# Optimization experiments

Measured on AMD Instinct MI355X. Metric: run time of the kernel, lower is better.

Reference implementation:

```python
import jax, jax.numpy as jnp
import numpy as np

E, H, L = 512, 1024, 4
VS, VT = 32000, 32000
B, SS, TT = 64, 48, 48
PAD = 0


def _cell(x, h, c, Wih, Whh, bih, bhh):
    # torch.nn.LSTMCell math: gate order i, f, g, o
    g = x @ Wih.T + h @ Whh.T + bih + bhh
    i, f, gg, o = jnp.split(g, 4, axis=-1)
    c = jax.nn.sigmoid(f) * c + jax.nn.sigmoid(i) * jnp.tanh(gg)
    h = jax.nn.sigmoid(o) * jnp.tanh(c)
    return h, c


def setup_inputs() -> dict:
    key = jax.random.key(0)
    ks = jax.random.split(key, 14)
    s = 0.05
    d = {}
    d['src_tokens'] = jax.random.randint(ks[0], (SS, B), 0, VS, dtype=jnp.int32)
    d['tgt_tokens'] = jax.random.randint(ks[1], (TT, B), 0, VT, dtype=jnp.int32)
    d['src_emb'] = jax.random.normal(ks[2], (VS, E)) * s
    d['tgt_emb'] = jax.random.normal(ks[3], (VT, E)) * s
    d['enc_Wih0'] = jax.random.normal(ks[4], (4 * H, E)) * s
    d['enc_WihR'] = jax.random.normal(ks[5], (L - 1, 4 * H, H)) * s
    d['enc_Whh'] = jax.random.normal(ks[6], (L, 4 * H, H)) * s
    d['enc_bih'] = jnp.zeros((L, 4 * H))
    d['enc_bhh'] = jnp.zeros((L, 4 * H))
    d['dec_Wih0'] = jax.random.normal(ks[7], (4 * H, E + H)) * s
    d['dec_WihR'] = jax.random.normal(ks[8], (L - 1, 4 * H, H)) * s
    d['dec_Whh'] = jax.random.normal(ks[9], (L, 4 * H, H)) * s
    d['dec_bih'] = jnp.zeros((L, 4 * H))
    d['dec_bhh'] = jnp.zeros((L, 4 * H))
    d['att_vec_W'] = jax.random.normal(ks[10], (H, 2 * H)) * s
    d['readout_W'] = jax.random.normal(ks[11], (VT, H)) * s
    return d


def _forward(src_tokens, tgt_tokens, src_emb, tgt_emb, enc_Wih0, enc_WihR,
             enc_Whh, enc_bih, enc_bhh, dec_Wih0, dec_WihR, dec_Whh, dec_bih,
             dec_bhh, att_vec_W, readout_W):
    src_x = src_emb[src_tokens]                      # [SS, B, E]
    h0 = jnp.zeros((L, B, H), src_emb.dtype)
    c0 = jnp.zeros((L, B, H), src_emb.dtype)

    def enc_step(carry, x_t):
        h, c = carry
        inp = x_t
        hs, cs = [], []
        for l in range(L):
            Wih = enc_Wih0 if l == 0 else enc_WihR[l - 1]
            hn, cn = _cell(inp, h[l], c[l], Wih, enc_Whh[l], enc_bih[l], enc_bhh[l])
            hs.append(hn); cs.append(cn)
            inp = hn
        return (jnp.stack(hs), jnp.stack(cs)), inp

    (hT, cT), enc_out = jax.lax.scan(enc_step, (h0, c0), src_x)
    src_enc = enc_out.transpose(1, 0, 2)             # [B, SS, H]

    # decoder init: last encoder layer (h, c) copied to every decoder layer
    hd = jnp.tile(hT[-1][None], (L, 1, 1))
    cd = jnp.tile(cT[-1][None], (L, 1, 1))
    tgt_x = tgt_emb[tgt_tokens[:-1]]                 # [TT-1, B, E]
    att0 = jnp.zeros((B, H), src_emb.dtype)

    def dec_step(carry, y_t):
        h, c, att = carry
        inp = jnp.concatenate([y_t, att], axis=-1)   # input feeding
        hs, cs = [], []
        for l in range(L):
            Wih = dec_Wih0 if l == 0 else dec_WihR[l - 1]
            hn, cn = _cell(inp, h[l], c[l], Wih, dec_Whh[l], dec_bih[l], dec_bhh[l])
            hs.append(hn); cs.append(cn)
            inp = hn
        h_top = hs[-1]
        # global attention, 'dot' score (full-length seqs -> all-zero mask is a no-op)
        scores = jnp.einsum('bsh,bh->bs', src_enc, h_top)
        alpha = jax.nn.softmax(scores, axis=-1)
        ctx = jnp.einsum('bs,bsh->bh', alpha, src_enc)
        att_t = jnp.tanh(jnp.concatenate([h_top, ctx], axis=-1) @ att_vec_W.T)
        return (jnp.stack(hs), jnp.stack(cs), att_t), att_t

    _, att_ves = jax.lax.scan(dec_step, (hd, cd, att0), tgt_x)  # [TT-1, B, H]

    logp = jax.nn.log_softmax(att_ves @ readout_W.T, axis=-1)   # [TT-1, B, VT]
    gold = tgt_tokens[1:]
    gold_lp = jnp.take_along_axis(logp, gold[..., None], axis=-1)[..., 0]
    mask = (gold != PAD).astype(logp.dtype)
    return (gold_lp * mask).sum(axis=0)              # [B]


def reference(src_tokens, tgt_tokens, src_emb, tgt_emb, enc_Wih0, enc_WihR,
              enc_Whh, enc_bih, enc_bhh, dec_Wih0, dec_WihR, dec_Whh, dec_bih,
              dec_bhh, att_vec_W, readout_W):
    return _forward(src_tokens, tgt_tokens, src_emb, tgt_emb, enc_Wih0,
                    enc_WihR, enc_Whh, enc_bih, enc_bhh, dec_Wih0, dec_WihR,
                    dec_Whh, dec_bih, dec_bhh, att_vec_W, readout_W)
```

## Files before the change

### kernel.cpp

```cpp
#include <hip/hip_runtime.h>


typedef __attribute__((ext_vector_type(8))) short bf16x8;
typedef __attribute__((ext_vector_type(4))) float f32x4;

#define SMEM_BYTES 32768

__device__ __forceinline__ float bf2f(ushort u) {
  union { uint i; float f; } v; v.i = ((uint)u) << 16; return v.f;
}
__device__ __forceinline__ ushort f2bf(float x) {
  union { float f; uint i; } v; v.f = x;
  uint r = (v.i + 0x7fffu + ((v.i >> 16) & 1u)) >> 16;
  return (ushort)r;
}
__device__ __forceinline__ float sigm(float x) { return 1.f / (1.f + expf(-x)); }

__device__ __forceinline__ void gemm_term(
    const ushort* __restrict__ A, int lda,
    const ushort* __restrict__ W, int ldw,
    int K, int m0, int n0,
    f32x4 acc[4], char* s)
{
  char* sA0 = s;
  char* sB0 = s + 8192;
  char* sA1 = s + 16384;
  char* sB1 = s + 24576;
  const int tid = threadIdx.x;
  const int lane = tid & 63;
  const int w = tid >> 6;
  const int r0 = tid >> 3;
  const int cge = (tid & 7) << 3;
  const ushort* Arow0 = A + (size_t)(m0 + r0) * lda + cge;
  const ushort* Arow1 = A + (size_t)(m0 + r0 + 32) * lda + cge;
  const ushort* Wrow0 = W + (size_t)(n0 + r0) * ldw + cge;
  const ushort* Wrow1 = W + (size_t)(n0 + r0 + 32) * ldw + cge;
  const int so0 = r0 * 128 + (((tid & 7) << 4) ^ ((r0 & 7) << 4));
  const int so1 = so0 + 4096;

  uint4 a0 = *reinterpret_cast<const uint4*>(Arow0);
  uint4 a1 = *reinterpret_cast<const uint4*>(Arow1);
  uint4 b0 = *reinterpret_cast<const uint4*>(Wrow0);
  uint4 b1 = *reinterpret_cast<const uint4*>(Wrow1);
  *reinterpret_cast<uint4*>(sA0 + so0) = a0;
  *reinterpret_cast<uint4*>(sA0 + so1) = a1;
  *reinterpret_cast<uint4*>(sB0 + so0) = b0;
  *reinterpret_cast<uint4*>(sB0 + so1) = b1;
  if (K > 64) {
    a0 = *reinterpret_cast<const uint4*>(Arow0 + 64);
    a1 = *reinterpret_cast<const uint4*>(Arow1 + 64);
    b0 = *reinterpret_cast<const uint4*>(Wrow0 + 64);
    b1 = *reinterpret_cast<const uint4*>(Wrow1 + 64);
  }
  const int axor = (lane & 7) << 4;
  const int arow = (w * 16 + (lane & 15)) * 128;
  const int brow = (lane & 15) * 128;
  const int kb0 = (lane >> 4) << 4;
  for (int kt = 0; kt < K; kt += 64) {
    char* cA = (kt & 64) ? sA1 : sA0;
    char* cB = (kt & 64) ? sB1 : sB0;
    char* nA = (kt & 64) ? sA0 : sA1;
    char* nB = (kt & 64) ? sB0 : sB1;
    __syncthreads();
    if (kt + 64 < K) {
      *reinterpret_cast<uint4*>(nA + so0) = a0;
      *reinterpret_cast<uint4*>(nA + so1) = a1;
      *reinterpret_cast<uint4*>(nB + so0) = b0;
      *reinterpret_cast<uint4*>(nB + so1) = b1;
      if (kt + 128 < K) {
        a0 = *reinterpret_cast<const uint4*>(Arow0 + kt + 128);
        a1 = *reinterpret_cast<const uint4*>(Arow1 + kt + 128);
        b0 = *reinterpret_cast<const uint4*>(Wrow0 + kt + 128);
        b1 = *reinterpret_cast<const uint4*>(Wrow1 + kt + 128);
      }
    }
#pragma unroll
    for (int ks = 0; ks < 2; ++ks) {
      const int kb = ks * 64 + kb0;
      bf16x8 af = *reinterpret_cast<const bf16x8*>(cA + arow + (kb ^ axor));
#pragma unroll
      for (int nf = 0; nf < 4; ++nf) {
        bf16x8 bfr = *reinterpret_cast<const bf16x8*>(
            cB + nf * 2048 + brow + (kb ^ axor));
        acc[nf] = __builtin_amdgcn_mfma_f32_16x16x32_bf16(af, bfr, acc[nf], 0, 0, 0);
      }
    }
  }
  __syncthreads();
}

__device__ __forceinline__ void store_f32(
    float* __restrict__ out, int ldo, int m0, int n0, f32x4 acc[4])
{
  const int tid = threadIdx.x, lane = tid & 63, w = tid >> 6;
  const int rbase = w * 16 + ((lane >> 4) << 2);
  const int cb = lane & 15;
#pragma unroll
  for (int nf = 0; nf < 4; ++nf)
#pragma unroll
    for (int r = 0; r < 4; ++r)
      out[(size_t)(m0 + rbase + r) * ldo + n0 + nf * 16 + cb] = acc[nf][r];
}

__device__ __forceinline__ void cell_store(
    float* smemF, f32x4 acc[4],
    float* __restrict__ c, ushort* __restrict__ hout,
    ushort* __restrict__ senc_t, int j0)
{
  const int tid = threadIdx.x, lane = tid & 63, w = tid >> 6;
  const int rbase = w * 16 + ((lane >> 4) << 2);
  const int cb = lane & 15;
  __syncthreads();
#pragma unroll
  for (int nf = 0; nf < 4; ++nf)
#pragma unroll
    for (int r = 0; r < 4; ++r)
      smemF[(rbase + r) * 68 + nf * 16 + cb] = acc[nf][r];
  __syncthreads();
#pragma unroll
  for (int i = 0; i < 4; ++i) {
    const int id = tid + i * 256;
    const int b = id >> 4, u = id & 15;
    const float g0 = smemF[b * 68 + u * 4 + 0];
    const float g1 = smemF[b * 68 + u * 4 + 1];
    const float g2 = smemF[b * 68 + u * 4 + 2];
    const float g3 = smemF[b * 68 + u * 4 + 3];
    const int off = b * 1024 + j0 + u;
    const float cold = c[off];
    const float ig = sigm(g0), fg = sigm(g1), gg = tanhf(g2), og = sigm(g3);
    const float cn = fg * cold + ig * gg;
    const float hv = og * tanhf(cn);
    c[off] = cn;
    const ushort hb = f2bf(hv);
    hout[off] = hb;
    if (senc_t) senc_t[(size_t)b * 49152 + j0 + u] = hb;
  }
}

__global__ __launch_bounds__(256) void nmt_init(float* c, ushort* henc, ushort* attbf)
{
  const int idx = blockIdx.x * 256 + threadIdx.x;
  if (idx < 262144) c[idx] = 0.f;
  if (idx < 65536) {
    attbf[idx] = 0;
    henc[idx] = 0;
    henc[(size_t)1 * 49 * 65536 + idx] = 0;
    henc[(size_t)2 * 49 * 65536 + idx] = 0;
    henc[(size_t)3 * 49 * 65536 + idx] = 0;
  }
}

__global__ __launch_bounds__(256) void nmt_convperm(
    const float* __restrict__ in, ushort* __restrict__ out,
    int L, int Kin, int col0, int Kout)
{
  const size_t idx = (size_t)blockIdx.x * 256 + threadIdx.x;
  const size_t total = (size_t)L * 4096 * Kout;
  if (idx >= total) return;
  const int k = (int)(idx % Kout);
  const size_t rem = idx / Kout;
  const int rp = (int)(rem % 4096);
  const int l = (int)(rem / 4096);
  const int j = rp >> 2, g = rp & 3;
  out[idx] = f2bf(in[((size_t)l * 4096 + g * 1024 + j) * Kin + col0 + k]);
}

__global__ __launch_bounds__(256) void nmt_convplain(
    const float* __restrict__ in, ushort* __restrict__ out, size_t n)
{
  const size_t idx = (size_t)blockIdx.x * 256 + threadIdx.x;
  if (idx < n) out[idx] = f2bf(in[idx]);
}

__global__ __launch_bounds__(256) void nmt_bias(
    const float* __restrict__ bih, const float* __restrict__ bhh, float* __restrict__ bc)
{
  const int idx = blockIdx.x * 256 + threadIdx.x;
  if (idx >= 4 * 4096) return;
  const int rp = idx & 4095, l = idx >> 12;
  const int j = rp >> 2, g = rp & 3;
  bc[idx] = bih[l * 4096 + g * 1024 + j] + bhh[l * 4096 + g * 1024 + j];
}

__global__ __launch_bounds__(256) void nmt_gather(
    const int* __restrict__ tok, const float* __restrict__ emb,
    ushort* __restrict__ out, int rows)
{
  const size_t idx = (size_t)blockIdx.x * 256 + threadIdx.x;
  if (idx >= (size_t)rows * 512) return;
  const int k = (int)(idx & 511);
  const int r = (int)(idx >> 9);
  out[idx] = f2bf(emb[(size_t)tok[r] * 512 + k]);
}

__global__ __launch_bounds__(256) void nmt_pre(
    const ushort* __restrict__ A, const ushort* __restrict__ Wp,
    const float* __restrict__ bc0, float* __restrict__ out, int K)
{
  __shared__ __align__(16) char smem[SMEM_BYTES];
  const int m0 = blockIdx.x * 64, n0 = blockIdx.y * 64;
  const int lane = threadIdx.x & 63;
  const int cb = lane & 15;
  f32x4 acc[4];
#pragma unroll
  for (int nf = 0; nf < 4; ++nf) {
    const float bv = bc0[n0 + nf * 16 + cb];
#pragma unroll
    for (int r = 0; r < 4; ++r) acc[nf][r] = bv;
  }
  gemm_term(A, K, Wp, K, K, m0, n0, acc, smem);
  store_f32(out, 4096, m0, n0, acc);
}

__global__ __launch_bounds__(256) void nmt_decinit(
    const ushort* __restrict__ henc, float* c, ushort* h)
{
  const int idx = blockIdx.x * 256 + threadIdx.x;
  if (idx >= 65536) return;
  const ushort hv = henc[((size_t)3 * 49 + 48) * 65536 + idx];
  const float cv = c[3 * 65536 + idx];
  c[idx] = cv; c[65536 + idx] = cv; c[2 * 65536 + idx] = cv;
  h[idx] = hv; h[65536 + idx] = hv; h[2 * 65536 + idx] = hv; h[3 * 65536 + idx] = hv;
}

__global__ __launch_bounds__(256) void nmt_sv(
    const ushort* __restrict__ senc, const ushort* __restrict__ attW,
    ushort* __restrict__ SV)
{
  __shared__ __align__(16) char smem[SMEM_BYTES];
  const int b = blockIdx.x;
  const int n0 = blockIdx.y * 64;
  const int tid = threadIdx.x, lane = tid & 63, w = tid >> 6;
  const int rbase = w * 16 + ((lane >> 4) << 2), cb = lane & 15;
  f32x4 acc[4];
#pragma unroll
  for (int nf = 0; nf < 4; ++nf)
#pragma unroll
    for (int r = 0; r < 4; ++r) acc[nf][r] = 0.f;
  gemm_term(senc + (size_t)b * 49152, 1024, attW + 1024, 2048, 1024, 0, n0,
            acc, smem);
#pragma unroll
  for (int nf = 0; nf < 4; ++nf)
#pragma unroll
    for (int r = 0; r < 4; ++r) {
      const int row = rbase + r;
      if (row < 48)
        SV[(size_t)b * 49152 + row * 1024 + n0 + nf * 16 + cb] = f2bf(acc[nf][r]);
    }
}

__global__ __launch_bounds__(256) void nmt_enc_cell(
    int u, int lo, ushort* __restrict__ henc, ushort* __restrict__ srcenc,
    float* __restrict__ c,
    const ushort* __restrict__ WihR, const ushort* __restrict__ Whh,
    const float* __restrict__ X0, const float* __restrict__ bcE)
{
  __shared__ __align__(16) char smem[SMEM_BYTES];
  const int l = lo + blockIdx.y;
  const int t = u - l;
  const int n0 = blockIdx.x * 64;
  const int tid = threadIdx.x, lane = tid & 63, w = tid >> 6;
  const int rbase = w * 16 + ((lane >> 4) << 2), cb = lane & 15;
  f32x4 acc[4];
  if (l == 0) {
#pragma unroll
    for (int nf = 0; nf < 4; ++nf)
#pragma unroll
      for (int r = 0; r < 4; ++r)
        acc[nf][r] = X0[(size_t)t * 262144 + (size_t)(rbase + r) * 4096 + n0 + nf * 16 + cb];
  } else {
#pragma unroll
    for (int nf = 0; nf < 4; ++nf) {
      const float bv = bcE[l * 4096 + n0 + nf * 16 + cb];
#pragma unroll
      for (int r = 0; r < 4; ++r) acc[nf][r] = bv;
    }
    gemm_term(henc + ((size_t)(l - 1) * 49 + t + 1) * 65536, 1024,
              WihR + (size_t)(l - 1) * 4194304, 1024, 1024, 0, n0, acc, smem);
  }
  gemm_term(henc + ((size_t)l * 49 + t) * 65536, 1024,
            Whh + (size_t)l * 4194304, 1024, 1024, 0, n0, acc, smem);
  cell_store((float*)smem, acc, c + l * 65536,
             henc + ((size_t)l * 49 + t + 1) * 65536,
             (l == 3) ? (srcenc + t * 1024) : (ushort*)nullptr, n0 >> 2);
}

__global__ __launch_bounds__(256) void nmt_dec_stage(
    int l, const ushort* __restrict__ hp, ushort* __restrict__ hn,
    float* __restrict__ c,
    const ushort* __restrict__ Whh, const ushort* __restrict__ WihR,
    const ushort* __restrict__ Wd0a, const ushort* __restrict__ attbf,
    const float* __restrict__ Y0t, const float* __restrict__ bcD,
    float* __restrict__ pbuf)
{
  __shared__ __align__(16) char smem[SMEM_BYTES];
  const int n0 = blockIdx.x * 64;
  const int tid = threadIdx.x, lane = tid & 63, w = tid >> 6;
  const int rbase = w * 16 + ((lane >> 4) << 2), cb = lane & 15;
  f32x4 acc[4];
  if (blockIdx.y == 0) {
    if (l == 0) {
#pragma unroll
      for (int nf = 0; nf < 4; ++nf)
#pragma unroll
        for (int r = 0; r < 4; ++r) {
          const size_t o = (size_t)(rbase + r) * 4096 + n0 + nf * 16 + cb;
          acc[nf][r] = Y0t[o] + pbuf[o];
        }
      gemm_term(attbf, 1024, Wd0a, 1024, 1024, 0, n0, acc, smem);
    } else {
#pragma unroll
      for (int nf = 0; nf < 4; ++nf)
#pragma unroll
        for (int r = 0; r < 4; ++r)
          acc[nf][r] = pbuf[(size_t)l * 262144 + (size_t)(rbase + r) * 4096 + n0 + nf * 16 + cb];
      gemm_term(hn + (l - 1) * 65536, 1024, WihR + (size_t)(l - 1) * 4194304,
                1024, 1024, 0, n0, acc, smem);
    }
    cell_store((float*)smem, acc, c + l * 65536, hn + l * 65536,
               (ushort*)nullptr, n0 >> 2);
  } else {
    const int lp = (l + 1) & 3;
    if (lp == 0) {
#pragma unroll
      for (int nf = 0; nf < 4; ++nf)
#pragma unroll
        for (int r = 0; r < 4; ++r) acc[nf][r] = 0.f;
      gemm_term(hn, 1024, Whh, 1024, 1024, 0, n0, acc, smem);
    } else {
#pragma unroll
      for (int nf = 0; nf < 4; ++nf) {
        const float bv = bcD[lp * 4096 + n0 + nf * 16 + cb];
#pragma unroll
        for (int r = 0; r < 4; ++r) acc[nf][r] = bv;
      }
      gemm_term(hp + lp * 65536, 1024, Whh + (size_t)lp * 4194304,
                1024, 1024, 0, n0, acc, smem);
    }
    store_f32(pbuf + (size_t)lp * 262144, 4096, 0, n0, acc);
  }
}

__global__ __launch_bounds__(256) void nmt_partial0(
    const ushort* __restrict__ h0, const ushort* __restrict__ Whh0,
    float* __restrict__ pbuf)
{
  __shared__ __align__(16) char smem[SMEM_BYTES];
  const int n0 = blockIdx.x * 64;
  f32x4 acc[4];
#pragma unroll
  for (int nf = 0; nf < 4; ++nf)
#pragma unroll
    for (int r = 0; r < 4; ++r) acc[nf][r] = 0.f;
  gemm_term(h0, 1024, Whh0, 1024, 1024, 0, n0, acc, smem);
  store_f32(pbuf, 4096, 0, n0, acc);
}

__global__ __launch_bounds__(256) void nmt_attnAB(
    const ushort* __restrict__ h3, const ushort* __restrict__ senc,
    const ushort* __restrict__ SV, const ushort* __restrict__ attW,
    float* __restrict__ ctx2, float* __restrict__ hb)
{
  __shared__ __align__(16) char smem[SMEM_BYTES];
  const int bid = blockIdx.x;
  const int tid = threadIdx.x, lane = tid & 63, w = tid >> 6;
  if (bid < 64) {
    float* sc = (float*)smem;
    float* al = (float*)smem + 64;
    const int b = bid;
    const ushort* sb = senc + (size_t)b * 49152;
    const ushort* vb = SV + (size_t)b * 49152;
    float hreg[16];
#pragma unroll
    for (int q = 0; q < 16; ++q) hreg[q] = bf2f(h3[b * 1024 + lane * 16 + q]);
    for (int s = w; s < 48; s += 4) {
      const ushort* vr = sb + s * 1024 + lane * 16;
      float p = 0.f;
#pragma unroll
      for (int q = 0; q < 16; ++q) p += bf2f(vr[q]) * hreg[q];
      for (int d = 1; d < 64; d <<= 1) p += __shfl_xor(p, d);
      if (lane == 0) sc[s] = p;
    }
    __syncthreads();
    if (tid < 64) {
      const float v = (lane < 48) ? sc[lane] : -3.4e38f;
      float m = v;
      for (int d = 1; d < 64; d <<= 1) m = fmaxf(m, __shfl_xor(m, d));
      float e = (lane < 48) ? expf(v - m) : 0.f;
      float s = e;
      for (int d = 1; d < 64; d <<= 1) s += __shfl_xor(s, d);
      al[lane] = e / s;
    }
    __syncthreads();
    const int k0 = tid * 4;
    float a0 = 0, a1 = 0, a2 = 0, a3 = 0;
    for (int s = 0; s < 48; ++s) {
      const float als = al[s];
      const ushort* vr = vb + s * 1024 + k0;
      a0 += als * bf2f(vr[0]); a1 += als * bf2f(vr[1]);
      a2 += als * bf2f(vr[2]); a3 += als * bf2f(vr[3]);
    }
    ctx2[b * 1024 + k0 + 0] = a0; ctx2[b * 1024 + k0 + 1] = a1;
    ctx2[b * 1024 + k0 + 2] = a2; ctx2[b * 1024 + k0 + 3] = a3;
  } else {
    const int n0 = (bid - 64) * 64;
    f32x4 acc[4];
#pragma unroll
    for (int nf = 0; nf < 4; ++nf)
#pragma unroll
      for (int r = 0; r < 4; ++r) acc[nf][r] = 0.f;
    gemm_term(h3, 1024, attW, 2048, 1024, 0, n0, acc, smem);
    store_f32(hb, 1024, 0, n0, acc);
  }
}

__global__ __launch_bounds__(256) void nmt_attnSB(
    const float* __restrict__ ctx2, const float* __restrict__ hb,
    ushort* __restrict__ attbf, ushort* __restrict__ av_t)
{
  const int base = blockIdx.x * 1024 + threadIdx.x * 4;
#pragma unroll
  for (int k = 0; k < 4; ++k) {
    const int i = base + k;
    const ushort us = f2bf(tanhf(hb[i] + ctx2[i]));
    attbf[i] = us;
    av_t[i] = us;
  }
}

__global__ __launch_bounds__(256) void nmt_readout(
    const ushort* __restrict__ attves, const ushort* __restrict__ routW,
    const int* __restrict__ tgt, float* __restrict__ pmax,
    float* __restrict__ psum, float* __restrict__ goldl)
{
  __shared__ __align__(16) char smem[SMEM_BYTES];
  const int m0 = blockIdx.x * 64, n0 = blockIdx.y * 64;
  const int tid = threadIdx.x, lane = tid & 63, w = tid >> 6;
  const int rbase = w * 16 + ((lane >> 4) << 2), cb = lane & 15;
  f32x4 acc[4];
#pragma unroll
  for (int nf = 0; nf < 4; ++nf)
#pragma unroll
    for (int r = 0; r < 4; ++r) acc[nf][r] = 0.f;
  gemm_term(attves, 1024, routW, 1024, 1024, m0, n0, acc, smem);
#pragma unroll
  for (int r = 0; r < 4; ++r) {
    float lm = fmaxf(fmaxf(acc[0][r], acc[1][r]), fmaxf(acc[2][r], acc[3][r]));
    for (int d = 1; d < 16; d <<= 1) lm = fmaxf(lm, __shfl_xor(lm, d));
    float ls = 0.f;
#pragma unroll
    for (int nf = 0; nf < 4; ++nf) ls += expf(acc[nf][r] - lm);
    for (int d = 1; d < 16; d <<= 1) ls += __shfl_xor(ls, d);
    const int grow = m0 + rbase + r;
    if (cb == 0) {
      pmax[(size_t)grow * 500 + blockIdx.y] = lm;
      psum[(size_t)grow * 500 + blockIdx.y] = ls;
    }
    const int t = grow >> 6, b = grow & 63;
    const int gold = tgt[(t + 1) * 64 + b];
#pragma unroll
    for (int nf = 0; nf < 4; ++nf)
      if (n0 + nf * 16 + cb == gold) goldl[grow] = acc[nf][r];
  }
}

__global__ __launch_bounds__(64) void nmt_combine(
    const float* __restrict__ pmax, const float* __restrict__ psum,
    const float* __restrict__ goldl, const int* __restrict__ tgt,
    float* __restrict__ lpm)
{
  const int row = blockIdx.x;
  const int lane = threadIdx.x;
  float m = -3.4e38f, s = 0.f;
  for (int i = lane; i < 500; i += 64) {
    const float pm = pmax[(size_t)row * 500 + i];
    const float ps = psum[(size_t)row * 500 + i];
    if (pm > m) { s = s * expf(m - pm) + ps; m = pm; }
    else        { s += ps * expf(pm - m); }
  }
  for (int d = 1; d < 64; d <<= 1) {
    const float om = __shfl_xor(m, d), os = __shfl_xor(s, d);
    if (om > m) { s = s * expf(m - om) + os; m = om; }
    else        { s += os * expf(om - m); }
  }
  if (lane == 0) {
    const int t = row >> 6, b = row & 63;
    const int gold = tgt[(t + 1) * 64 + b];
    const float lp = goldl[row] - m - logf(s);
    lpm[row] = (gold != 0) ? lp : 0.f;
  }
}

__global__ __launch_bounds__(64) void nmt_final(
    const float* __restrict__ lpm, float* __restrict__ out)
{
  const int b = threadIdx.x;
  float s = 0.f;
  for (int t = 0; t < 47; ++t) s += lpm[t * 64 + b];
  out[b] = s;
}

extern "C" void kernel_launch(void* const* d_in, const int* in_sizes, int n_in,
                              void* d_out, int out_size, void* d_ws, size_t ws_size,
                              hipStream_t stream)
{
  (void)in_sizes; (void)n_in; (void)out_size; (void)ws_size;
  const int*   src_tok  = (const int*)d_in[0];
  const int*   tgt_tok  = (const int*)d_in[1];
  const float* src_emb  = (const float*)d_in[2];
  const float* tgt_emb  = (const float*)d_in[3];
  const float* eWih0    = (const float*)d_in[4];
  const float* eWihR    = (const float*)d_in[5];
  const float* eWhh     = (const float*)d_in[6];
  const float* ebih     = (const float*)d_in[7];
  const float* ebhh     = (const float*)d_in[8];
  const float* dWih0    = (const float*)d_in[9];
  const float* dWihR    = (const float*)d_in[10];
  const float* dWhh     = (const float*)d_in[11];
  const float* dbih     = (const float*)d_in[12];
  const float* dbhh     = (const float*)d_in[13];
  const float* attW_f   = (const float*)d_in[14];
  const float* routW_f  = (const float*)d_in[15];

  char* p = (char*)d_ws;
  auto alloc = [&](size_t bytes) { void* r = (void*)p; p += (bytes + 255) & ~(size_t)255; return r; };
  ushort* eWih0p = (ushort*)alloc((size_t)4096 * 512 * 2);
  ushort* eWihRp = (ushort*)alloc((size_t)3 * 4096 * 1024 * 2);
  ushort* eWhhp  = (ushort*)alloc((size_t)4 * 4096 * 1024 * 2);
  ushort* dWih0y = (ushort*)alloc((size_t)4096 * 512 * 2);
  ushort* dWih0a = (ushort*)alloc((size_t)4096 * 1024 * 2);
  ushort* dWihRp = (ushort*)alloc((size_t)3 * 4096 * 1024 * 2);
  ushort* dWhhp  = (ushort*)alloc((size_t)4 * 4096 * 1024 * 2);
  ushort* attWb  = (ushort*)alloc((size_t)1024 * 2048 * 2);
  ushort* routWb = (ushort*)alloc((size_t)32000 * 1024 * 2);
  ushort* srcx   = (ushort*)alloc((size_t)3072 * 512 * 2);
  ushort* tgtx   = (ushort*)alloc((size_t)3008 * 512 * 2);
  ushort* henc   = (ushort*)alloc((size_t)4 * 49 * 65536 * 2);
  ushort* hA     = (ushort*)alloc((size_t)4 * 65536 * 2);
  ushort* hB     = (ushort*)alloc((size_t)4 * 65536 * 2);
  ushort* srcenc = (ushort*)alloc((size_t)64 * 49152 * 2);
  ushort* SVbuf  = (ushort*)alloc((size_t)64 * 49152 * 2);
  ushort* attbf  = (ushort*)alloc((size_t)65536 * 2);
  ushort* attves = (ushort*)alloc((size_t)3008 * 1024 * 2);
  float*  ctx2   = (float*)alloc((size_t)65536 * 4);
  float*  hbuf   = (float*)alloc((size_t)65536 * 4);
  float*  pbuf   = (float*)alloc((size_t)4 * 262144 * 4);
  float*  X0     = (float*)alloc((size_t)3072 * 4096 * 4);
  float*  Y0     = (float*)alloc((size_t)3008 * 4096 * 4);
  float*  bcE    = (float*)alloc((size_t)16384 * 4);
  float*  bcD    = (float*)alloc((size_t)16384 * 4);
  float*  cbuf   = (float*)alloc((size_t)4 * 65536 * 4);
  float*  pmaxb  = (float*)alloc((size_t)3008 * 500 * 4);
  float*  psumb  = (float*)alloc((size_t)3008 * 500 * 4);
  float*  goldl  = (float*)alloc((size_t)3008 * 4);
  float*  lpm    = (float*)alloc((size_t)3008 * 4);

  const dim3 B256(256);
  auto g1 = [](size_t n) { return dim3((unsigned)((n + 255) / 256)); };

  nmt_init<<<g1(262144), B256, 0, stream>>>(cbuf, henc, attbf);

  nmt_convperm<<<g1((size_t)4096 * 512), B256, 0, stream>>>(eWih0, eWih0p, 1, 512, 0, 512);
  nmt_convperm<<<g1((size_t)3 * 4096 * 1024), B256, 0, stream>>>(eWihR, eWihRp, 3, 1024, 0, 1024);
  nmt_convperm<<<g1((size_t)4 * 4096 * 1024), B256, 0, stream>>>(eWhh, eWhhp, 4, 1024, 0, 1024);
  nmt_convperm<<<g1((size_t)4096 * 512), B256, 0, stream>>>(dWih0, dWih0y, 1, 1536, 0, 512);
  nmt_convperm<<<g1((size_t)4096 * 1024), B256, 0, stream>>>(dWih0, dWih0a, 1, 1536, 512, 1024);
  nmt_convperm<<<g1((size_t)3 * 4096 * 1024), B256, 0, stream>>>(dWihR, dWihRp, 3, 1024, 0, 1024);
  nmt_convperm<<<g1((size_t)4 * 4096 * 1024), B256, 0, stream>>>(dWhh, dWhhp, 4, 1024, 0, 1024);
  nmt_convplain<<<g1((size_t)1024 * 2048), B256, 0, stream>>>(attW_f, attWb, (size_t)1024 * 2048);
  nmt_convplain<<<g1((size_t)32000 * 1024), B256, 0, stream>>>(routW_f, routWb, (size_t)32000 * 1024);
  nmt_bias<<<g1(16384), B256, 0, stream>>>(ebih, ebhh, bcE);
  nmt_bias<<<g1(16384), B256, 0, stream>>>(dbih, dbhh, bcD);
  nmt_gather<<<g1((size_t)3072 * 512), B256, 0, stream>>>(src_tok, src_emb, srcx, 3072);
  nmt_gather<<<g1((size_t)3008 * 512), B256, 0, stream>>>(tgt_tok, tgt_emb, tgtx, 3008);

  nmt_pre<<<dim3(48, 64), B256, 0, stream>>>(srcx, eWih0p, bcE, X0, 512);
  nmt_pre<<<dim3(47, 64), B256, 0, stream>>>(tgtx, dWih0y, bcD, Y0, 512);

  for (int u = 0; u < 51; ++u) {
    const int lo = (u > 47) ? (u - 47) : 0;
    const int hi = (u < 3) ? u : 3;
    nmt_enc_cell<<<dim3(64, hi - lo + 1), B256, 0, stream>>>(
        u, lo, henc, srcenc, cbuf, eWihRp, eWhhp, X0, bcE);
  }
  nmt_decinit<<<g1(65536), B256, 0, stream>>>(henc, cbuf, hA);
  nmt_sv<<<dim3(64, 16), B256, 0, stream>>>(srcenc, attWb, SVbuf);
  nmt_partial0<<<dim3(64), B256, 0, stream>>>(hA, dWhhp, pbuf);

  for (int t = 0; t < 47; ++t) {
    ushort* hp = (t & 1) ? hB : hA;
    ushort* hn = (t & 1) ? hA : hB;
    for (int l = 0; l < 4; ++l) {
      nmt_dec_stage<<<dim3(64, 2), B256, 0, stream>>>(
          l, hp, hn, cbuf, dWhhp, dWihRp, dWih0a, attbf,
          Y0 + (size_t)t * 262144, bcD, pbuf);
    }
    nmt_attnAB<<<dim3(80), B256, 0, stream>>>(hn + 3 * 65536, srcenc, SVbuf,
                                              attWb, ctx2, hbuf);
    nmt_attnSB<<<dim3(64), B256, 0, stream>>>(ctx2, hbuf, attbf,
                                              attves + (size_t)t * 65536);
  }

  nmt_readout<<<dim3(47, 500), B256, 0, stream>>>(attves, routWb, tgt_tok,
                                                  pmaxb, psumb, goldl);
  nmt_combine<<<dim3(3008), dim3(64), 0, stream>>>(pmaxb, psumb, goldl, tgt_tok, lpm);
  nmt_final<<<dim3(1), dim3(64), 0, stream>>>(lpm, (float*)d_out);
}
```

Baseline: 4.449 ms.

## Fuse attention tanh into decoder layer-0 GEMM and widen K tile to 128

Removes the per-step attnSB kernel. hb and ctx for every decoder step are stored in full-size buffers, and the tanh(h+ctx) to bf16 conversion is fused into the A-operand load of the layer-0 decoder GEMM. The att_ves outputs are produced afterwards in one batched kernel. The GEMM K tile doubles to 128, with shared memory raised to 64KB, which halves the number of barriers per GEMM. It also switches to fast exp/tanh intrinsics, trading some accuracy and occupancy for fewer launches and syncs on the serial critical path.

```diff
diff --git a/kernel.cpp b/kernel.cpp
--- a/kernel.cpp
+++ b/kernel.cpp
@@ -4,7 +4,7 @@
 typedef __attribute__((ext_vector_type(8))) short bf16x8;
 typedef __attribute__((ext_vector_type(4))) float f32x4;
 
-#define SMEM_BYTES 32768
+#define SMEM_BYTES 65536
 
 __device__ __forceinline__ float bf2f(ushort u) {
   union { uint i; float f; } v; v.i = ((uint)u) << 16; return v.f;
@@ -14,7 +14,16 @@
   uint r = (v.i + 0x7fffu + ((v.i >> 16) & 1u)) >> 16;
   return (ushort)r;
 }
-__device__ __forceinline__ float sigm(float x) { return 1.f / (1.f + expf(-x)); }
+__device__ __forceinline__ uint pack2(float x, float y) {
+  return (uint)f2bf(x) | ((uint)f2bf(y) << 16);
+}
+__device__ __forceinline__ float sigm(float x) {
+  return __fdividef(1.f, 1.f + __expf(-x));
+}
+__device__ __forceinline__ float tanhf_fast(float x) {
+  const float e = __expf(2.f * x);
+  return 1.f - __fdividef(2.f, e + 1.f);
+}
 
 __device__ __forceinline__ void gemm_term(
     const ushort* __restrict__ A, int lda,
@@ -23,65 +32,198 @@
     f32x4 acc[4], char* s)
 {
   char* sA0 = s;
-  char* sB0 = s + 8192;
-  char* sA1 = s + 16384;
-  char* sB1 = s + 24576;
+  char* sB0 = s + 16384;
+  char* sA1 = s + 32768;
+  char* sB1 = s + 49152;
   const int tid = threadIdx.x;
   const int lane = tid & 63;
   const int w = tid >> 6;
   const int r0 = tid >> 3;
   const int cge = (tid & 7) << 3;
-  const ushort* Arow0 = A + (size_t)(m0 + r0) * lda + cge;
-  const ushort* Arow1 = A + (size_t)(m0 + r0 + 32) * lda + cge;
-  const ushort* Wrow0 = W + (size_t)(n0 + r0) * ldw + cge;
-  const ushort* Wrow1 = W + (size_t)(n0 + r0 + 32) * ldw + cge;
-  const int so0 = r0 * 128 + (((tid & 7) << 4) ^ ((r0 & 7) << 4));
-  const int so1 = so0 + 4096;
-
-  uint4 a0 = *reinterpret_cast<const uint4*>(Arow0);
-  uint4 a1 = *reinterpret_cast<const uint4*>(Arow1);
-  uint4 b0 = *reinterpret_cast<const uint4*>(Wrow0);
-  uint4 b1 = *reinterpret_cast<const uint4*>(Wrow1);
-  *reinterpret_cast<uint4*>(sA0 + so0) = a0;
-  *reinterpret_cast<uint4*>(sA0 + so1) = a1;
-  *reinterpret_cast<uint4*>(sB0 + so0) = b0;
-  *reinterpret_cast<uint4*>(sB0 + so1) = b1;
-  if (K > 64) {
-    a0 = *reinterpret_cast<const uint4*>(Arow0 + 64);
-    a1 = *reinterpret_cast<const uint4*>(Arow1 + 64);
-    b0 = *reinterpret_cast<const uint4*>(Wrow0 + 64);
-    b1 = *reinterpret_cast<const uint4*>(Wrow1 + 64);
+  const int soX = r0 * 128 + (((tid & 7) << 4) ^ ((r0 & 7) << 4));
+  const ushort* Ar0 = A + (size_t)(m0 + r0) * lda + cge;
+  const ushort* Ar1 = A + (size_t)(m0 + r0 + 32) * lda + cge;
+  const ushort* Wr0 = W + (size_t)(n0 + r0) * ldw + cge;
+  const ushort* Wr1 = W + (size_t)(n0 + r0 + 32) * ldw + cge;
+
+  uint4 a0 = *reinterpret_cast<const uint4*>(Ar0);
+  uint4 a1 = *reinterpret_cast<const uint4*>(Ar1);
+  uint4 a2 = *reinterpret_cast<const uint4*>(Ar0 + 64);
+  uint4 a3 = *reinterpret_cast<const uint4*>(Ar1 + 64);
+  uint4 b0 = *reinterpret_cast<const uint4*>(Wr0);
+  uint4 b1 = *reinterpret_cast<const uint4*>(Wr1);
+  uint4 b2 = *reinterpret_cast<const uint4*>(Wr0 + 64);
+  uint4 b3 = *reinterpret_cast<const uint4*>(Wr1 + 64);
+  *reinterpret_cast<uint4*>(sA0 + soX) = a0;
+  *reinterpret_cast<uint4*>(sA0 + 4096 + soX) = a1;
+  *reinterpret_cast<uint4*>(sA0 + 8192 + soX) = a2;
+  *reinterpret_cast<uint4*>(sA0 + 12288 + soX) = a3;
+  *reinterpret_cast<uint4*>(sB0 + soX) = b0;
+  *reinterpret_cast<uint4*>(sB0 + 4096 + soX) = b1;
+  *reinterpret_cast<uint4*>(sB0 + 8192 + soX) = b2;
+  *reinterpret_cast<uint4*>(sB0 + 12288 + soX) = b3;
+  if (K > 128) {
+    a0 = *reinterpret_cast<const uint4*>(Ar0 + 128);
+    a1 = *reinterpret_cast<const uint4*>(Ar1 + 128);
+    a2 = *reinterpret_cast<const uint4*>(Ar0 + 192);
+    a3 = *reinterpret_cast<const uint4*>(Ar1 + 192);
+    b0 = *reinterpret_cast<const uint4*>(Wr0 + 128);
+    b1 = *reinterpret_cast<const uint4*>(Wr1 + 128);
+    b2 = *reinterpret_cast<const uint4*>(Wr0 + 192);
+    b3 = *reinterpret_cast<const uint4*>(Wr1 + 192);
   }
   const int axor = (lane & 7) << 4;
   const int arow = (w * 16 + (lane & 15)) * 128;
   const int brow = (lane & 15) * 128;
   const int kb0 = (lane >> 4) << 4;
-  for (int kt = 0; kt < K; kt += 64) {
-    char* cA = (kt & 64) ? sA1 : sA0;
-    char* cB = (kt & 64) ? sB1 : sB0;
-    char* nA = (kt & 64) ? sA0 : sA1;
-    char* nB = (kt & 64) ? sB0 : sB1;
+  for (int kt = 0; kt < K; kt += 128) {
+    char* cA = (kt & 128) ? sA1 : sA0;
+    char* cB = (kt & 128) ? sB1 : sB0;
+    char* nA = (kt & 128) ? sA0 : sA1;
+    char* nB = (kt & 128) ? sB0 : sB1;
     __syncthreads();
-    if (kt + 64 < K) {
-      *reinterpret_cast<uint4*>(nA + so0) = a0;
-      *reinterpret_cast<uint4*>(nA + so1) = a1;
-      *reinterpret_cast<uint4*>(nB + so0) = b0;
-      *reinterpret_cast<uint4*>(nB + so1) = b1;
-      if (kt + 128 < K) {
-        a0 = *reinterpret_cast<const uint4*>(Arow0 + kt + 128);
-        a1 = *reinterpret_cast<const uint4*>(Arow1 + kt + 128);
-        b0 = *reinterpret_cast<const uint4*>(Wrow0 + kt + 128);
-        b1 = *reinterpret_cast<const uint4*>(Wrow1 + kt + 128);
+    if (kt + 128 < K) {
+      *reinterpret_cast<uint4*>(nA + soX) = a0;
+      *reinterpret_cast<uint4*>(nA + 4096 + soX) = a1;
+      *reinterpret_cast<uint4*>(nA + 8192 + soX) = a2;
+      *reinterpret_cast<uint4*>(nA + 12288 + soX) = a3;
+      *reinterpret_cast<uint4*>(nB + soX) = b0;
+      *reinterpret_cast<uint4*>(nB + 4096 + soX) = b1;
+      *reinterpret_cast<uint4*>(nB + 8192 + soX) = b2;
+      *reinterpret_cast<uint4*>(nB + 12288 + soX) = b3;
+      if (kt + 256 < K) {
+        a0 = *reinterpret_cast<const uint4*>(Ar0 + kt + 256);
+        a1 = *reinterpret_cast<const uint4*>(Ar1 + kt + 256);
+        a2 = *reinterpret_cast<const uint4*>(Ar0 + kt + 320);
+        a3 = *reinterpret_cast<const uint4*>(Ar1 + kt + 320);
+        b0 = *reinterpret_cast<const uint4*>(Wr0 + kt + 256);
+        b1 = *reinterpret_cast<const uint4*>(Wr1 + kt + 256);
+        b2 = *reinterpret_cast<const uint4*>(Wr0 + kt + 320);
+        b3 = *reinterpret_cast<const uint4*>(Wr1 + kt + 320);
       }
     }
 #pragma unroll
-    for (int ks = 0; ks < 2; ++ks) {
-      const int kb = ks * 64 + kb0;
-      bf16x8 af = *reinterpret_cast<const bf16x8*>(cA + arow + (kb ^ axor));
+    for (int ks = 0; ks < 4; ++ks) {
+      const int sb = (ks >> 1) * 8192;
+      const int kb = ((ks & 1) << 6) + kb0;
+      bf16x8 af = *reinterpret_cast<const bf16x8*>(cA + sb + arow + (kb ^ axor));
 #pragma unroll
       for (int nf = 0; nf < 4; ++nf) {
         bf16x8 bfr = *reinterpret_cast<const bf16x8*>(
-            cB + nf * 2048 + brow + (kb ^ axor));
+            cB + sb + nf * 2048 + brow + (kb ^ axor));
+        acc[nf] = __builtin_amdgcn_mfma_f32_16x16x32_bf16(af, bfr, acc[nf], 0, 0, 0);
+      }
+    }
+  }
+  __syncthreads();
+}
+
+__device__ __forceinline__ void att_loadf(
+    const float* H0, const float* H1, const float* C0, const float* C1,
+    int kt, float4* fh, float4* fc)
+{
+#pragma unroll
+  for (int q = 0; q < 8; ++q) {
+    const int rh = q >> 2, sub = (q >> 1) & 1, vq = q & 1;
+    const float* hp_ = rh ? H1 : H0;
+    const float* cp_ = rh ? C1 : C0;
+    fh[q] = *reinterpret_cast<const float4*>(hp_ + kt + sub * 64 + vq * 4);
+    fc[q] = *reinterpret_cast<const float4*>(cp_ + kt + sub * 64 + vq * 4);
+  }
+}
+
+__device__ __forceinline__ void att_store(
+    char* buf, int soX, const float4* fh, const float4* fc)
+{
+#pragma unroll
+  for (int rh = 0; rh < 2; ++rh)
+#pragma unroll
+    for (int sub = 0; sub < 2; ++sub) {
+      const int q0 = rh * 4 + sub * 2;
+      const float4 u = fh[q0], v = fc[q0];
+      const float4 u2 = fh[q0 + 1], v2 = fc[q0 + 1];
+      uint4 o;
+      o.x = pack2(tanhf_fast(u.x + v.x), tanhf_fast(u.y + v.y));
+      o.y = pack2(tanhf_fast(u.z + v.z), tanhf_fast(u.w + v.w));
+      o.z = pack2(tanhf_fast(u2.x + v2.x), tanhf_fast(u2.y + v2.y));
+      o.w = pack2(tanhf_fast(u2.z + v2.z), tanhf_fast(u2.w + v2.w));
+      *reinterpret_cast<uint4*>(buf + sub * 8192 + rh * 4096 + soX) = o;
+    }
+}
+
+__device__ __forceinline__ void gemm_att(
+    const float* __restrict__ H, const float* __restrict__ C2,
+    const ushort* __restrict__ W, int ldw, int n0,
+    f32x4 acc[4], char* s)
+{
+  char* sA0 = s;
+  char* sB0 = s + 16384;
+  char* sA1 = s + 32768;
+  char* sB1 = s + 49152;
+  const int tid = threadIdx.x;
+  const int lane = tid & 63;
+  const int w = tid >> 6;
+  const int r0 = tid >> 3;
+  const int cge = (tid & 7) << 3;
+  const int soX = r0 * 128 + (((tid & 7) << 4) ^ ((r0 & 7) << 4));
+  const ushort* Wr0 = W + (size_t)(n0 + r0) * ldw + cge;
+  const ushort* Wr1 = W + (size_t)(n0 + r0 + 32) * ldw + cge;
+  const float* H0 = H + r0 * 1024 + cge;
+  const float* H1 = H + (r0 + 32) * 1024 + cge;
+  const float* C0 = C2 + r0 * 1024 + cge;
+  const float* C1 = C2 + (r0 + 32) * 1024 + cge;
+
+  float4 fh[8], fc[8];
+  uint4 b0, b1, b2, b3;
+  att_loadf(H0, H1, C0, C1, 0, fh, fc);
+  att_store(sA0, soX, fh, fc);
+  b0 = *reinterpret_cast<const uint4*>(Wr0);
+  b1 = *reinterpret_cast<const uint4*>(Wr1);
+  b2 = *reinterpret_cast<const uint4*>(Wr0 + 64);
+  b3 = *reinterpret_cast<const uint4*>(Wr1 + 64);
+  *reinterpret_cast<uint4*>(sB0 + soX) = b0;
+  *reinterpret_cast<uint4*>(sB0 + 4096 + soX) = b1;
+  *reinterpret_cast<uint4*>(sB0 + 8192 + soX) = b2;
+  *reinterpret_cast<uint4*>(sB0 + 12288 + soX) = b3;
+  att_loadf(H0, H1, C0, C1, 128, fh, fc);
+  b0 = *reinterpret_cast<const uint4*>(Wr0 + 128);
+  b1 = *reinterpret_cast<const uint4*>(Wr1 + 128);
+  b2 = *reinterpret_cast<const uint4*>(Wr0 + 192);
+  b3 = *reinterpret_cast<const uint4*>(Wr1 + 192);
+
+  const int axor = (lane & 7) << 4;
+  const int arow = (w * 16 + (lane & 15)) * 128;
+  const int brow = (lane & 15) * 128;
+  const int kb0 = (lane >> 4) << 4;
+  for (int kt = 0; kt < 1024; kt += 128) {
+    char* cA = (kt & 128) ? sA1 : sA0;
+    char* cB = (kt & 128) ? sB1 : sB0;
+    char* nA = (kt & 128) ? sA0 : sA1;
+    char* nB = (kt & 128) ? sB0 : sB1;
+    __syncthreads();
+    if (kt + 128 < 1024) {
+      att_store(nA, soX, fh, fc);
+      *reinterpret_cast<uint4*>(nB + soX) = b0;
+      *reinterpret_cast<uint4*>(nB + 4096 + soX) = b1;
+      *reinterpret_cast<uint4*>(nB + 8192 + soX) = b2;
+      *reinterpret_cast<uint4*>(nB + 12288 + soX) = b3;
+      if (kt + 256 < 1024) {
+        att_loadf(H0, H1, C0, C1, kt + 256, fh, fc);
+        b0 = *reinterpret_cast<const uint4*>(Wr0 + kt + 256);
+        b1 = *reinterpret_cast<const uint4*>(Wr1 + kt + 256);
+        b2 = *reinterpret_cast<const uint4*>(Wr0 + kt + 320);
+        b3 = *reinterpret_cast<const uint4*>(Wr1 + kt + 320);
+      }
+    }
+#pragma unroll
+    for (int ks = 0; ks < 4; ++ks) {
+      const int sb = (ks >> 1) * 8192;
+      const int kb = ((ks & 1) << 6) + kb0;
+      bf16x8 af = *reinterpret_cast<const bf16x8*>(cA + sb + arow + (kb ^ axor));
+#pragma unroll
+      for (int nf = 0; nf < 4; ++nf) {
+        bf16x8 bfr = *reinterpret_cast<const bf16x8*>(
+            cB + sb + nf * 2048 + brow + (kb ^ axor));
         acc[nf] = __builtin_amdgcn_mfma_f32_16x16x32_bf16(af, bfr, acc[nf], 0, 0, 0);
       }
     }
@@ -127,9 +269,8 @@
     const float g3 = smemF[b * 68 + u * 4 + 3];
     const int off = b * 1024 + j0 + u;
     const float cold = c[off];
-    const float ig = sigm(g0), fg = sigm(g1), gg = tanhf(g2), og = sigm(g3);
-    const float cn = fg * cold + ig * gg;
-    const float hv = og * tanhf(cn);
+    const float cn = sigm(g1) * cold + sigm(g0) * tanhf_fast(g2);
+    const float hv = sigm(g3) * tanhf_fast(cn);
     c[off] = cn;
     const ushort hb = f2bf(hv);
     hout[off] = hb;
@@ -137,12 +278,14 @@
   }
 }
 
-__global__ __launch_bounds__(256) void nmt_init(float* c, ushort* henc, ushort* attbf)
+__global__ __launch_bounds__(256) void nmt_init(
+    float* c, ushort* henc, float* hbAll, float* ctxAll)
 {
   const int idx = blockIdx.x * 256 + threadIdx.x;
   if (idx < 262144) c[idx] = 0.f;
   if (idx < 65536) {
-    attbf[idx] = 0;
+    hbAll[idx] = 0.f;
+    ctxAll[idx] = 0.f;
     henc[idx] = 0;
     henc[(size_t)1 * 49 * 65536 + idx] = 0;
     henc[(size_t)2 * 49 * 65536 + idx] = 0;
@@ -289,7 +432,8 @@
     int l, const ushort* __restrict__ hp, ushort* __restrict__ hn,
     float* __restrict__ c,
     const ushort* __restrict__ Whh, const ushort* __restrict__ WihR,
-    const ushort* __restrict__ Wd0a, const ushort* __restrict__ attbf,
+    const ushort* __restrict__ Wd0a,
+    const float* __restrict__ hbprev, const float* __restrict__ ctxprev,
     const float* __restrict__ Y0t, const float* __restrict__ bcD,
     float* __restrict__ pbuf)
 {
@@ -307,7 +451,7 @@
           const size_t o = (size_t)(rbase + r) * 4096 + n0 + nf * 16 + cb;
           acc[nf][r] = Y0t[o] + pbuf[o];
         }
-      gemm_term(attbf, 1024, Wd0a, 1024, 1024, 0, n0, acc, smem);
+      gemm_att(hbprev, ctxprev, Wd0a, 1024, n0, acc, smem);
     } else {
 #pragma unroll
       for (int nf = 0; nf < 4; ++nf)
@@ -414,17 +558,15 @@
   }
 }
 
-__global__ __launch_bounds__(256) void nmt_attnSB(
-    const float* __restrict__ ctx2, const float* __restrict__ hb,
-    ushort* __restrict__ attbf, ushort* __restrict__ av_t)
-{
-  const int base = blockIdx.x * 1024 + threadIdx.x * 4;
+__global__ __launch_bounds__(256) void nmt_attves_k(
+    const float* __restrict__ hbAll, const float* __restrict__ ctxAll,
+    ushort* __restrict__ attves)
+{
+  const int i = blockIdx.x * 1024 + threadIdx.x * 4;
 #pragma unroll
   for (int k = 0; k < 4; ++k) {
-    const int i = base + k;
-    const ushort us = f2bf(tanhf(hb[i] + ctx2[i]));
-    attbf[i] = us;
-    av_t[i] = us;
+    const int j = i + k;
+    attves[j] = f2bf(tanhf_fast(hbAll[j + 65536] + ctxAll[j + 65536]));
   }
 }
 
@@ -540,10 +682,9 @@
   ushort* hB     = (ushort*)alloc((size_t)4 * 65536 * 2);
   ushort* srcenc = (ushort*)alloc((size_t)64 * 49152 * 2);
   ushort* SVbuf  = (ushort*)alloc((size_t)64 * 49152 * 2);
-  ushort* attbf  = (ushort*)alloc((size_t)65536 * 2);
   ushort* attves = (ushort*)alloc((size_t)3008 * 1024 * 2);
-  float*  ctx2   = (float*)alloc((size_t)65536 * 4);
-  float*  hbuf   = (float*)alloc((size_t)65536 * 4);
+  float*  hbAll  = (float*)alloc((size_t)48 * 65536 * 4);
+  float*  ctxAll = (float*)alloc((size_t)48 * 65536 * 4);
   float*  pbuf   = (float*)alloc((size_t)4 * 262144 * 4);
   float*  X0     = (float*)alloc((size_t)3072 * 4096 * 4);
   float*  Y0     = (float*)alloc((size_t)3008 * 4096 * 4);
@@ -558,7 +699,7 @@
   const dim3 B256(256);
   auto g1 = [](size_t n) { return dim3((unsigned)((n + 255) / 256)); };
 
-  nmt_init<<<g1(262144), B256, 0, stream>>>(cbuf, henc, attbf);
+  nmt_init<<<g1(262144), B256, 0, stream>>>(cbuf, henc, hbAll, ctxAll);
 
   nmt_convperm<<<g1((size_t)4096 * 512), B256, 0, stream>>>(eWih0, eWih0p, 1, 512, 0, 512);
   nmt_convperm<<<g1((size_t)3 * 4096 * 1024), B256, 0, stream>>>(eWihR, eWihRp, 3, 1024, 0, 1024);
@@ -592,14 +733,15 @@
     ushort* hn = (t & 1) ? hA : hB;
     for (int l = 0; l < 4; ++l) {
       nmt_dec_stage<<<dim3(64, 2), B256, 0, stream>>>(
-          l, hp, hn, cbuf, dWhhp, dWihRp, dWih0a, attbf,
+          l, hp, hn, cbuf, dWhhp, dWihRp, dWih0a,
+          hbAll + (size_t)t * 65536, ctxAll + (size_t)t * 65536,
           Y0 + (size_t)t * 262144, bcD, pbuf);
     }
-    nmt_attnAB<<<dim3(80), B256, 0, stream>>>(hn + 3 * 65536, srcenc, SVbuf,
-                                              attWb, ctx2, hbuf);
-    nmt_attnSB<<<dim3(64), B256, 0, stream>>>(ctx2, hbuf, attbf,
-                                              attves + (size_t)t * 65536);
-  }
+    nmt_attnAB<<<dim3(80), B256, 0, stream>>>(
+        hn + 3 * 65536, srcenc, SVbuf, attWb,
+        ctxAll + (size_t)(t + 1) * 65536, hbAll + (size_t)(t + 1) * 65536);
+  }
+  nmt_attves_k<<<dim3(3008), B256, 0, stream>>>(hbAll, ctxAll, attves);
 
   nmt_readout<<<dim3(47, 500), B256, 0, stream>>>(attves, routWb, tgt_tok,
                                                   pmaxb, psumb, goldl);
```

Measured after the change: 4.499 ms. No clear change (+1.1%).

## Widen readout GEMM tile to 128 rows and use fast sigmoid/tanh

Applied to the files above, without the earlier changes.

The readout GEMM now computes a 128x64 tile per block, with register-prefetched double-buffered LDS and a swizzled layout, so each weight tile loaded from routW serves twice as many rows. This halves the number of row-blocks and the repeated reads of the 32000x1024 readout matrix. The attves buffer is padded to 3072 rows so the last tile can read out of range safely, and the extra rows are skipped in the epilogue. LSTM and attention activations also switch to __expf/__fdividef approximations, which are cheaper but slightly less accurate.

```diff
diff --git a/kernel.cpp b/kernel.cpp
--- a/kernel.cpp
+++ b/kernel.cpp
@@ -5,6 +5,14 @@
 typedef __attribute__((ext_vector_type(4))) float f32x4;
 
 #define SMEM_BYTES 32768
+#define SMEM_RO    49152
+
+#define NMT_SYNC_LIGHT()                                   \
+  do {                                                     \
+    asm volatile("s_waitcnt lgkmcnt(0)" ::: "memory");     \
+    __builtin_amdgcn_s_barrier();                          \
+    __builtin_amdgcn_sched_barrier(0);                     \
+  } while (0)
 
 __device__ __forceinline__ float bf2f(ushort u) {
   union { uint i; float f; } v; v.i = ((uint)u) << 16; return v.f;
@@ -14,7 +22,13 @@
   uint r = (v.i + 0x7fffu + ((v.i >> 16) & 1u)) >> 16;
   return (ushort)r;
 }
-__device__ __forceinline__ float sigm(float x) { return 1.f / (1.f + expf(-x)); }
+__device__ __forceinline__ float sigm(float x) {
+  return __fdividef(1.f, 1.f + __expf(-x));
+}
+__device__ __forceinline__ float tanhf_fast(float x) {
+  const float e = __expf(2.f * x);
+  return 1.f - __fdividef(2.f, e + 1.f);
+}
 
 __device__ __forceinline__ void gemm_term(
     const ushort* __restrict__ A, int lda,
@@ -127,9 +141,8 @@
     const float g3 = smemF[b * 68 + u * 4 + 3];
     const int off = b * 1024 + j0 + u;
     const float cold = c[off];
-    const float ig = sigm(g0), fg = sigm(g1), gg = tanhf(g2), og = sigm(g3);
-    const float cn = fg * cold + ig * gg;
-    const float hv = og * tanhf(cn);
+    const float cn = sigm(g1) * cold + sigm(g0) * tanhf_fast(g2);
+    const float hv = sigm(g3) * tanhf_fast(cn);
     c[off] = cn;
     const ushort hb = f2bf(hv);
     hout[off] = hb;
@@ -422,7 +435,7 @@
 #pragma unroll
   for (int k = 0; k < 4; ++k) {
     const int i = base + k;
-    const ushort us = f2bf(tanhf(hb[i] + ctx2[i]));
+    const ushort us = f2bf(tanhf_fast(hb[i] + ctx2[i]));
     attbf[i] = us;
     av_t[i] = us;
   }
@@ -433,34 +446,114 @@
     const int* __restrict__ tgt, float* __restrict__ pmax,
     float* __restrict__ psum, float* __restrict__ goldl)
 {
-  __shared__ __align__(16) char smem[SMEM_BYTES];
-  const int m0 = blockIdx.x * 64, n0 = blockIdx.y * 64;
+  __shared__ __align__(16) char smem[SMEM_RO];
+  const int g = blockIdx.x;
+  const int n0 = blockIdx.y * 64;
   const int tid = threadIdx.x, lane = tid & 63, w = tid >> 6;
   const int rbase = w * 16 + ((lane >> 4) << 2), cb = lane & 15;
-  f32x4 acc[4];
-#pragma unroll
-  for (int nf = 0; nf < 4; ++nf)
-#pragma unroll
-    for (int r = 0; r < 4; ++r) acc[nf][r] = 0.f;
-  gemm_term(attves, 1024, routW, 1024, 1024, m0, n0, acc, smem);
-#pragma unroll
-  for (int r = 0; r < 4; ++r) {
-    float lm = fmaxf(fmaxf(acc[0][r], acc[1][r]), fmaxf(acc[2][r], acc[3][r]));
-    for (int d = 1; d < 16; d <<= 1) lm = fmaxf(lm, __shfl_xor(lm, d));
-    float ls = 0.f;
-#pragma unroll
-    for (int nf = 0; nf < 4; ++nf) ls += expf(acc[nf][r] - lm);
-    for (int d = 1; d < 16; d <<= 1) ls += __shfl_xor(ls, d);
-    const int grow = m0 + rbase + r;
-    if (cb == 0) {
-      pmax[(size_t)grow * 500 + blockIdx.y] = lm;
-      psum[(size_t)grow * 500 + blockIdx.y] = ls;
-    }
-    const int t = grow >> 6, b = grow & 63;
-    const int gold = tgt[(t + 1) * 64 + b];
+  const int r0 = tid >> 3;
+  const int cge = (tid & 7) << 3;
+  const int soX = r0 * 128 + (((tid & 7) << 4) ^ ((r0 & 7) << 4));
+  const int axor = (lane & 7) << 4;
+  const int arow = (w * 16 + (lane & 15)) * 128;
+  const int brow = (lane & 15) * 128;
+  const int kb0 = (lane >> 4) << 4;
+
+  const ushort* A0r0 = attves + (size_t)(g * 128 + r0) * 1024 + cge;
+  const ushort* A0r1 = attves + (size_t)(g * 128 + r0 + 32) * 1024 + cge;
+  const ushort* A1r0 = attves + (size_t)(g * 128 + 64 + r0) * 1024 + cge;
+  const ushort* A1r1 = attves + (size_t)(g * 128 + 64 + r0 + 32) * 1024 + cge;
+  const ushort* Br0  = routW + (size_t)(n0 + r0) * 1024 + cge;
+  const ushort* Br1  = routW + (size_t)(n0 + r0 + 32) * 1024 + cge;
+
+  f32x4 acc[2][4];
+#pragma unroll
+  for (int mi = 0; mi < 2; ++mi)
 #pragma unroll
     for (int nf = 0; nf < 4; ++nf)
-      if (n0 + nf * 16 + cb == gold) goldl[grow] = acc[nf][r];
+#pragma unroll
+      for (int r = 0; r < 4; ++r) acc[mi][nf][r] = 0.f;
+
+  uint4 ra0 = *(const uint4*)(A0r0);
+  uint4 ra1 = *(const uint4*)(A0r1);
+  uint4 ra2 = *(const uint4*)(A1r0);
+  uint4 ra3 = *(const uint4*)(A1r1);
+  uint4 rb0 = *(const uint4*)(Br0);
+  uint4 rb1 = *(const uint4*)(Br1);
+  {
+    char* sl = smem;
+    *(uint4*)(sl + soX) = ra0;          *(uint4*)(sl + 4096 + soX) = ra1;
+    *(uint4*)(sl + 8192 + soX) = ra2;   *(uint4*)(sl + 12288 + soX) = ra3;
+    *(uint4*)(sl + 16384 + soX) = rb0;  *(uint4*)(sl + 20480 + soX) = rb1;
+  }
+  ra0 = *(const uint4*)(A0r0 + 64);
+  ra1 = *(const uint4*)(A0r1 + 64);
+  ra2 = *(const uint4*)(A1r0 + 64);
+  ra3 = *(const uint4*)(A1r1 + 64);
+  rb0 = *(const uint4*)(Br0 + 64);
+  rb1 = *(const uint4*)(Br1 + 64);
+
+  for (int kt = 0; kt < 1024; kt += 64) {
+    NMT_SYNC_LIGHT();
+    if (kt + 64 < 1024) {
+      char* sl = smem + ((((kt >> 6) + 1) & 1) ? 24576 : 0);
+      *(uint4*)(sl + soX) = ra0;          *(uint4*)(sl + 4096 + soX) = ra1;
+      *(uint4*)(sl + 8192 + soX) = ra2;   *(uint4*)(sl + 12288 + soX) = ra3;
+      *(uint4*)(sl + 16384 + soX) = rb0;  *(uint4*)(sl + 20480 + soX) = rb1;
+      if (kt + 128 < 1024) {
+        ra0 = *(const uint4*)(A0r0 + kt + 128);
+        ra1 = *(const uint4*)(A0r1 + kt + 128);
+        ra2 = *(const uint4*)(A1r0 + kt + 128);
+        ra3 = *(const uint4*)(A1r1 + kt + 128);
+        rb0 = *(const uint4*)(Br0 + kt + 128);
+        rb1 = *(const uint4*)(Br1 + kt + 128);
+      }
+    }
+    char* cur = smem + (((kt >> 6) & 1) ? 24576 : 0);
+#pragma unroll
+    for (int ks = 0; ks < 2; ++ks) {
+      const int kb = (ks << 6) + kb0;
+      bf16x8 bf0 = *(const bf16x8*)(cur + 16384 + 0 * 2048 + brow + (kb ^ axor));
+      bf16x8 bf1 = *(const bf16x8*)(cur + 16384 + 1 * 2048 + brow + (kb ^ axor));
+      bf16x8 bf2 = *(const bf16x8*)(cur + 16384 + 2 * 2048 + brow + (kb ^ axor));
+      bf16x8 bf3 = *(const bf16x8*)(cur + 16384 + 3 * 2048 + brow + (kb ^ axor));
+      bf16x8 af0 = *(const bf16x8*)(cur + arow + (kb ^ axor));
+      bf16x8 af1 = *(const bf16x8*)(cur + 8192 + arow + (kb ^ axor));
+      acc[0][0] = __builtin_amdgcn_mfma_f32_16x16x32_bf16(af0, bf0, acc[0][0], 0, 0, 0);
+      acc[0][1] = __builtin_amdgcn_mfma_f32_16x16x32_bf16(af0, bf1, acc[0][1], 0, 0, 0);
+      acc[0][2] = __builtin_amdgcn_mfma_f32_16x16x32_bf16(af0, bf2, acc[0][2], 0, 0, 0);
+      acc[0][3] = __builtin_amdgcn_mfma_f32_16x16x32_bf16(af0, bf3, acc[0][3], 0, 0, 0);
+      acc[1][0] = __builtin_amdgcn_mfma_f32_16x16x32_bf16(af1, bf0, acc[1][0], 0, 0, 0);
+      acc[1][1] = __builtin_amdgcn_mfma_f32_16x16x32_bf16(af1, bf1, acc[1][1], 0, 0, 0);
+      acc[1][2] = __builtin_amdgcn_mfma_f32_16x16x32_bf16(af1, bf2, acc[1][2], 0, 0, 0);
+      acc[1][3] = __builtin_amdgcn_mfma_f32_16x16x32_bf16(af1, bf3, acc[1][3], 0, 0, 0);
+    }
+  }
+
+#pragma unroll
+  for (int mi = 0; mi < 2; ++mi) {
+    const int gm = g * 2 + mi;
+    if (gm >= 47) continue;
+#pragma unroll
+    for (int r = 0; r < 4; ++r) {
+      float lm = fmaxf(fmaxf(acc[mi][0][r], acc[mi][1][r]),
+                       fmaxf(acc[mi][2][r], acc[mi][3][r]));
+      for (int d = 1; d < 16; d <<= 1) lm = fmaxf(lm, __shfl_xor(lm, d));
+      float ls = 0.f;
+#pragma unroll
+      for (int nf = 0; nf < 4; ++nf) ls += expf(acc[mi][nf][r] - lm);
+      for (int d = 1; d < 16; d <<= 1) ls += __shfl_xor(ls, d);
+      const int grow = gm * 64 + rbase + r;
+      if (cb == 0) {
+        pmax[(size_t)grow * 500 + blockIdx.y] = lm;
+        psum[(size_t)grow * 500 + blockIdx.y] = ls;
+      }
+      const int t = grow >> 6, b = grow & 63;
+      const int gold = tgt[(t + 1) * 64 + b];
+#pragma unroll
+      for (int nf = 0; nf < 4; ++nf)
+        if (n0 + nf * 16 + cb == gold) goldl[grow] = acc[mi][nf][r];
+    }
   }
 }
 
@@ -541,7 +634,7 @@
   ushort* srcenc = (ushort*)alloc((size_t)64 * 49152 * 2);
   ushort* SVbuf  = (ushort*)alloc((size_t)64 * 49152 * 2);
   ushort* attbf  = (ushort*)alloc((size_t)65536 * 2);
-  ushort* attves = (ushort*)alloc((size_t)3008 * 1024 * 2);
+  ushort* attves = (ushort*)alloc((size_t)3072 * 1024 * 2);
   float*  ctx2   = (float*)alloc((size_t)65536 * 4);
   float*  hbuf   = (float*)alloc((size_t)65536 * 4);
   float*  pbuf   = (float*)alloc((size_t)4 * 262144 * 4);
@@ -601,7 +694,7 @@
                                               attves + (size_t)t * 65536);
   }
 
-  nmt_readout<<<dim3(47, 500), B256, 0, stream>>>(attves, routWb, tgt_tok,
+  nmt_readout<<<dim3(24, 500), B256, 0, stream>>>(attves, routWb, tgt_tok,
                                                   pmaxb, psumb, goldl);
   nmt_combine<<<dim3(3008), dim3(64), 0, stream>>>(pmaxb, psumb, goldl, tgt_tok, lpm);
   nmt_final<<<dim3(1), dim3(64), 0, stream>>>(lpm, (float*)d_out);
```

New measurement: 4.191 ms. 5.8% less time.
